# Performance work log

Measured on AMD Instinct MI355X. Metric: run time of the kernel, lower is better.

The kernel has to match this reference:

```python
import jax, jax.numpy as jnp
import numpy as np

N_NODES = 100000
N_EDGES = 1600000
N_FEAT = 128
HIDDEN = 128
N_GRAPHS = 64
N_CLASSES = 10
BN_EPS = 1e-5


def setup_inputs() -> dict:
    key = jax.random.key(0)
    ks = jax.random.split(key, 24)
    glorot = lambda k, o, i: jax.random.normal(k, (o, i), jnp.float32) * (1.0 / np.sqrt(i))
    inp = {
        'x': jax.random.normal(ks[0], (N_NODES, N_FEAT), jnp.float32),
        'edge_index': jax.random.randint(ks[1], (2, N_EDGES), 0, N_NODES, jnp.int64),
        'batch': jnp.sort(jax.random.randint(ks[2], (N_NODES,), 0, N_GRAPHS, jnp.int64)),
        # GCNConv(128 -> 128)
        'gcn_w': glorot(ks[3], HIDDEN, N_FEAT),
        'gcn_b': jnp.zeros((HIDDEN,), jnp.float32),
        # SAGEConv layers 1, 2: lin_l (aggregated, with bias) + lin_r (root, no bias)
        'sage1_wl': glorot(ks[4], HIDDEN, HIDDEN),
        'sage1_bl': jnp.zeros((HIDDEN,), jnp.float32),
        'sage1_wr': glorot(ks[5], HIDDEN, HIDDEN),
        'sage2_wl': glorot(ks[6], HIDDEN, HIDDEN),
        'sage2_bl': jnp.zeros((HIDDEN,), jnp.float32),
        'sage2_wr': glorot(ks[7], HIDDEN, HIDDEN),
        # ClassifierBase: 128 -> 200 -> 100 -> 50 -> 10
        'clf_w0': glorot(ks[8], 200, HIDDEN), 'clf_b0': jnp.zeros((200,), jnp.float32),
        'clf_w1': glorot(ks[9], 100, 200), 'clf_b1': jnp.zeros((100,), jnp.float32),
        'clf_w2': glorot(ks[10], 50, 100), 'clf_b2': jnp.zeros((50,), jnp.float32),
        'clf_w3': glorot(ks[11], N_CLASSES, 50), 'clf_b3': jnp.zeros((N_CLASSES,), jnp.float32),
        # BatchNorm1d (eval mode, running_mean=0, running_var=1)
        'bn0_g': jnp.ones((200,), jnp.float32), 'bn0_b': jnp.zeros((200,), jnp.float32),
        'bn1_g': jnp.ones((100,), jnp.float32), 'bn1_b': jnp.zeros((100,), jnp.float32),
        'bn2_g': jnp.ones((50,), jnp.float32), 'bn2_b': jnp.zeros((50,), jnp.float32),
    }
    return inp


def _gcn_conv(x, src, dst, W, b):
    # PyG GCNConv: add self loops, symmetric deg^{-1/2} normalization
    xw = x @ W.T                                                  # [N, H]
    ones = jnp.ones(src.shape[0], xw.dtype)
    deg = jax.ops.segment_sum(ones, dst, num_segments=N_NODES) + 1.0  # self loops
    dinv = jax.lax.rsqrt(deg)
    norm = dinv[src] * dinv[dst]                                  # [E]
    out = jax.ops.segment_sum(xw[src] * norm[:, None], dst, num_segments=N_NODES)
    out = out + xw * (dinv * dinv)[:, None]                       # self-loop term deg^{-1}
    return out + b


def _sage_conv(x, src, dst, Wl, bl, Wr):
    # PyG SAGEConv (mean aggr): lin_l(mean_{j->i} x_j) + lin_r(x_i)
    ones = jnp.ones(src.shape[0], x.dtype)
    cnt = jax.ops.segment_sum(ones, dst, num_segments=N_NODES)
    agg = jax.ops.segment_sum(x[src], dst, num_segments=N_NODES)
    agg = agg / jnp.maximum(cnt, 1.0)[:, None]
    return agg @ Wl.T + bl + x @ Wr.T


def _bn_eval(h, g, b):
    # eval-mode BatchNorm1d with running_mean=0, running_var=1
    return h * (g / np.sqrt(1.0 + BN_EPS)) + b


def reference(x, edge_index, batch, gcn_w, gcn_b,
              sage1_wl, sage1_bl, sage1_wr, sage2_wl, sage2_bl, sage2_wr,
              clf_w0, clf_b0, clf_w1, clf_b1, clf_w2, clf_b2, clf_w3, clf_b3,
              bn0_g, bn0_b, bn1_g, bn1_b, bn2_g, bn2_b):
    src, dst = edge_index[0], edge_index[1]
    h = _gcn_conv(x, src, dst, gcn_w, gcn_b)          # act_func is None -> no activation
    h = _sage_conv(h, src, dst, sage1_wl, sage1_bl, sage1_wr)
    h = _sage_conv(h, src, dst, sage2_wl, sage2_bl, sage2_wr)
    # global mean pool over graphs
    gcnt = jax.ops.segment_sum(jnp.ones(h.shape[0], h.dtype), batch, num_segments=N_GRAPHS)
    g = jax.ops.segment_sum(h, batch, num_segments=N_GRAPHS) / jnp.maximum(gcnt, 1.0)[:, None]
    # ClassifierBase (eval: dropout inactive), tanh activation
    g = jnp.tanh(_bn_eval(g @ clf_w0.T + clf_b0, bn0_g, bn0_b))
    g = jnp.tanh(_bn_eval(g @ clf_w1.T + clf_b1, bn1_g, bn1_b))
    g = jnp.tanh(_bn_eval(g @ clf_w2.T + clf_b2, bn2_g, bn2_b))
    logits = g @ clf_w3.T + clf_b3
    return jax.nn.softmax(logits, axis=1)             # [B, n_classes]
```

## Files before the change

### kernel.cpp

```cpp
#include <hip/hip_runtime.h>

#define N_NODES 100000
#define N_EDGES 1600000
#define NGRAPH 64
#define NBIN 391
#define EPB 2560
#define NBLK 625
#define CAPB 6144
#define CAPP 7168
#define PSPLIT 8

typedef short s8v __attribute__((ext_vector_type(8)));
typedef float f4v __attribute__((ext_vector_type(4)));
typedef float f2v __attribute__((ext_vector_type(2)));

__device__ __forceinline__ float bflo(unsigned u) { return __uint_as_float(u << 16); }
__device__ __forceinline__ float bfhi(unsigned u) { return __uint_as_float(u & 0xffff0000u); }
__device__ __forceinline__ unsigned short f2bf(float f) {
    unsigned u = __float_as_uint(f);
    u += 0x7fffu + ((u >> 16) & 1u);
    return (unsigned short)(u >> 16);
}
__device__ __forceinline__ float bf2f(unsigned short h) { return __uint_as_float(((unsigned)h) << 16); }
__device__ __forceinline__ unsigned pk(float lo, float hi) {
    return (unsigned)f2bf(lo) | ((unsigned)f2bf(hi) << 16);
}
__device__ __forceinline__ float ldv(const void* p, int i, int f32) {
    return f32 ? ((const float*)p)[i] : bf2f(((const unsigned short*)p)[i]);
}
__device__ __forceinline__ f2v up2(unsigned u) {
    f2v t; t.x = bflo(u); t.y = bfhi(u); return t;
}

__global__ __launch_bounds__(256) void k_setup(const unsigned short* __restrict__ x,
                                               const int* __restrict__ ei,
                                               const int* __restrict__ batch,
                                               int* __restrict__ flags,
                                               int* __restrict__ binCur,
                                               int* __restrict__ gstart,
                                               float* __restrict__ pbuf,
                                               float* __restrict__ wbuf,
                                               const void* w0, const void* w1,
                                               const void* w2, const void* w3,
                                               const void* b0, const void* bn0g, const void* bn0b,
                                               const void* b1, const void* bn1g, const void* bn1b,
                                               const void* b2, const void* bn2g, const void* bn2b,
                                               const void* b3) {
    __shared__ int cnt[3];
    int tid = threadIdx.x, bid = blockIdx.x;
    if (tid < 3) cnt[tid] = 0;
    __syncthreads();
    unsigned short h = x[tid * 37];
    int e = (h >> 7) & 0xFF;
    if (e >= 100 && e <= 150) atomicAdd(&cnt[0], 1);
    if (bid == 0) {
        if (ei[2 * (tid * 5000) + 1] == 0) atomicAdd(&cnt[1], 1);
        if (batch[2 * (tid * 193) + 1] == 0) atomicAdd(&cnt[2], 1);
    }
    __syncthreads();
    int f = (cnt[0] == 256) ? 0 : 1;
    int i = bid * 256 + tid;
    if (i < 25600) wbuf[i] = ldv(w0, i, f);
    else if (i < 45600) wbuf[i] = ldv(w1, i - 25600, f);
    else if (i < 50600) wbuf[i] = ldv(w2, i - 45600, f);
    else if (i < 51100) wbuf[i] = ldv(w3, i - 50600, f);
    if (bid != 0) return;
    int b64 = (cnt[2] == 256) ? 1 : 0;
    if (tid == 0) {
        flags[0] = f;
        flags[1] = (cnt[1] == 256) ? 1 : 0;
        flags[2] = b64;
    }
    for (int k = tid; k < NBIN; k += 256) binCur[k] = k * CAPB;
    if (tid <= NGRAPH) {
        int g = tid, lo = 0, hi = N_NODES;
        while (lo < hi) {
            int mid = (lo + hi) >> 1;
            int v = b64 ? batch[2 * mid] : batch[mid];
            if (v < g) lo = mid + 1;
            else hi = mid;
        }
        gstart[g] = lo;
    }
    const float invs = rsqrtf(1.0f + 1e-5f);
    if (tid < 200) {
        float a = ldv(bn0g, tid, f) * invs;
        pbuf[tid] = a;
        pbuf[200 + tid] = ldv(b0, tid, f) * a + ldv(bn0b, tid, f);
    }
    if (tid < 100) {
        float a = ldv(bn1g, tid, f) * invs;
        pbuf[400 + tid] = a;
        pbuf[500 + tid] = ldv(b1, tid, f) * a + ldv(bn1b, tid, f);
    }
    if (tid < 50) {
        float a = ldv(bn2g, tid, f) * invs;
        pbuf[600 + tid] = a;
        pbuf[650 + tid] = ldv(b2, tid, f) * a + ldv(bn2b, tid, f);
    }
    if (tid < 10) pbuf[700 + tid] = ldv(b3, tid, f);
}

__global__ __launch_bounds__(256) void k_binfill(const int* __restrict__ ei,
                                                 int* __restrict__ binCur,
                                                 unsigned* __restrict__ staging,
                                                 const int* __restrict__ flags) {
    __shared__ int cnt[NBIN];
    __shared__ int lofs[NBIN];
    __shared__ int curL[NBIN];
    __shared__ int basg[NBIN];
    __shared__ int sA[512], sB[512];
    __shared__ int sbuf[EPB];
    __shared__ int dbuf[EPB];
    __shared__ unsigned ebuf[EPB];
    __shared__ unsigned short bbuf[EPB];
    int tid = threadIdx.x;
    int i64 = flags[1];
    int base = blockIdx.x * EPB;
    for (int i = tid; i < NBIN; i += 256) cnt[i] = 0;
    __syncthreads();
    #pragma unroll
    for (int k = 0; k < EPB / 512; ++k) {
        int e = base + k * 512 + tid * 2;
        int s0, s1, d0, d1;
        if (i64) {
            uint4 vs = *(const uint4*)(ei + 2 * (size_t)e);
            uint4 vd = *(const uint4*)(ei + 2 * (size_t)(N_EDGES + e));
            s0 = (int)vs.x; s1 = (int)vs.z;
            d0 = (int)vd.x; d1 = (int)vd.z;
        } else {
            int2 vs = *(const int2*)(ei + (size_t)e);
            int2 vd = *(const int2*)(ei + (size_t)N_EDGES + e);
            s0 = vs.x; s1 = vs.y;
            d0 = vd.x; d1 = vd.y;
        }
        int l = k * 512 + tid * 2;
        sbuf[l] = s0; sbuf[l + 1] = s1;
        dbuf[l] = d0; dbuf[l + 1] = d1;
        if ((unsigned)d0 < N_NODES) atomicAdd(&cnt[d0 >> 8], 1);
        if ((unsigned)d1 < N_NODES) atomicAdd(&cnt[d1 >> 8], 1);
    }
    __syncthreads();
    for (int k = tid; k < 512; k += 256) sA[k] = (k < NBIN) ? cnt[k] : 0;
    __syncthreads();
    int* src = sA;
    int* dst = sB;
    for (int off = 1; off < 512; off <<= 1) {
        for (int k = tid; k < 512; k += 256)
            dst[k] = src[k] + ((k >= off) ? src[k - off] : 0);
        __syncthreads();
        int* t = src; src = dst; dst = t;
    }
    int totE = src[NBIN - 1];
    for (int i = tid; i < NBIN; i += 256) {
        int excl = src[i] - cnt[i];
        lofs[i] = excl;
        curL[i] = excl;
        basg[i] = cnt[i] ? atomicAdd(&binCur[i], cnt[i]) : 0;
    }
    __syncthreads();
    #pragma unroll
    for (int k = 0; k < EPB / 256; ++k) {
        int l = k * 256 + tid;
        int d = dbuf[l];
        int s = sbuf[l];
        if ((unsigned)d < N_NODES) {
            s = min(max(s, 0), N_NODES - 1);
            int p = atomicAdd(&curL[d >> 8], 1);
            ebuf[p] = ((unsigned)(d & 255) << 20) | (unsigned)s;
            bbuf[p] = (unsigned short)(d >> 8);
        }
    }
    __syncthreads();
    for (int i = tid; i < totE; i += 256) {
        int bb = bbuf[i];
        int p = basg[bb] + (i - lofs[bb]);
        if (p < (bb + 1) * CAPB) staging[p] = ebuf[i];
    }
}

__global__ __launch_bounds__(256) void k_csr(const unsigned* __restrict__ staging,
                                             const int* __restrict__ binCur,
                                             int2* __restrict__ rse,
                                             float* __restrict__ dinv,
                                             int* __restrict__ colidx,
                                             unsigned* __restrict__ padA,
                                             unsigned* __restrict__ padB) {
    __shared__ int deg[256];
    __shared__ int s[256];
    __shared__ int cur[256];
    __shared__ int colbuf[CAPP];
    int b = blockIdx.x, tid = threadIdx.x;
    int n0 = b << 8;
    int nend = min(256, N_NODES - n0);
    int runStart = b * CAPB;
    int outStart = b * CAPP;
    int runLen = min(binCur[b] - runStart, CAPB);
    deg[tid] = 0;
    for (int i = tid; i < CAPP; i += 256) colbuf[i] = N_NODES;
    __syncthreads();
    for (int i = tid; i < runLen; i += 256)
        atomicAdd(&deg[staging[runStart + i] >> 20], 1);
    __syncthreads();
    int myDeg = deg[tid];
    int pdeg = (myDeg + 15) & ~15;
    s[tid] = pdeg;
    __syncthreads();
    for (int off = 1; off < 256; off <<= 1) {
        int x2 = (tid >= off) ? s[tid - off] : 0;
        __syncthreads();
        s[tid] += x2;
        __syncthreads();
    }
    int incl = s[tid];
    int lrs = incl - pdeg;
    if (tid < nend) {
        rse[n0 + tid] = make_int2(outStart + lrs, outStart + lrs + myDeg);
        dinv[n0 + tid] = rsqrtf((float)myDeg + 1.0f);
    }
    cur[tid] = lrs;
    __syncthreads();
    for (int i = tid; i < runLen; i += 256) {
        unsigned e = staging[runStart + i];
        int p = atomicAdd(&cur[e >> 20], 1);
        if (p < CAPP) colbuf[p] = (int)(e & 0xFFFFF);
    }
    __syncthreads();
    int ptot = min(s[255], CAPP);
    for (int i = tid; i < ptot; i += 256) colidx[outStart + i] = colbuf[i];
    if (b == 0) {
        if (tid < 64) {
            padA[(size_t)N_NODES * 64 + tid] = 0u;
            padB[(size_t)N_NODES * 64 + tid] = 0u;
        }
        if (tid == 0) dinv[N_NODES] = 0.f;
    }
}

__global__ __launch_bounds__(256) void k_cvtx(const void* __restrict__ src,
                                              unsigned* __restrict__ out,
                                              const int* __restrict__ flags) {
    if (!flags[0]) return;
    int id = blockIdx.x * 256 + threadIdx.x;
    if (id >= N_NODES * 64) return;
    float2 u = ((const float2*)src)[id];
    out[id] = pk(u.x, u.y);
}

template <int MODE>
__global__ __launch_bounds__(256) void k_agg(const uint4* __restrict__ xsA,
                                             const uint4* __restrict__ xsB,
                                             const int2* __restrict__ rse,
                                             const float* __restrict__ dinv,
                                             unsigned* __restrict__ out,
                                             const int* __restrict__ col,
                                             const int* __restrict__ flags) {
    int lane = threadIdx.x & 63;
    int node = blockIdx.x * 4 + (threadIdx.x >> 6);
    int glane = lane & 15, grp = lane >> 4;
    const uint4* xs = (MODE == 0) ? (flags[0] ? xsB : xsA) : xsA;
    int2 rr = rse[node];
    int rs = rr.x, deg = rr.y - rr.x;
    int pend = rs + ((deg + 15) & ~15);
    f2v a0 = {0.f, 0.f}, a1 = {0.f, 0.f}, a2 = {0.f, 0.f}, a3 = {0.f, 0.f};
    uint4 selfu = make_uint4(0u, 0u, 0u, 0u);
    float di = 0.f;
    if (MODE == 0) {
        selfu = xs[(unsigned)node * 16u + glane];
        di = dinv[node];
    }

    for (int base = rs; base < pend; base += 16) {
        int4 c = *(const int4*)(col + base + grp * 4);
        float dv0, dv1, dv2, dv3;
        if (MODE == 0) {
            dv0 = dinv[c.x]; dv1 = dinv[c.y]; dv2 = dinv[c.z]; dv3 = dinv[c.w];
            c.x = min(c.x, N_NODES - 1); c.y = min(c.y, N_NODES - 1);
            c.z = min(c.z, N_NODES - 1); c.w = min(c.w, N_NODES - 1);
        }
        uint4 u0 = xs[(unsigned)c.x * 16u + glane];
        uint4 u1 = xs[(unsigned)c.y * 16u + glane];
        uint4 u2 = xs[(unsigned)c.z * 16u + glane];
        uint4 u3 = xs[(unsigned)c.w * 16u + glane];
        if (MODE == 0) {
            a0 += dv0 * up2(u0.x); a1 += dv0 * up2(u0.y); a2 += dv0 * up2(u0.z); a3 += dv0 * up2(u0.w);
            a0 += dv1 * up2(u1.x); a1 += dv1 * up2(u1.y); a2 += dv1 * up2(u1.z); a3 += dv1 * up2(u1.w);
            a0 += dv2 * up2(u2.x); a1 += dv2 * up2(u2.y); a2 += dv2 * up2(u2.z); a3 += dv2 * up2(u2.w);
            a0 += dv3 * up2(u3.x); a1 += dv3 * up2(u3.y); a2 += dv3 * up2(u3.z); a3 += dv3 * up2(u3.w);
        } else {
            a0 += up2(u0.x); a1 += up2(u0.y); a2 += up2(u0.z); a3 += up2(u0.w);
            a0 += up2(u1.x); a1 += up2(u1.y); a2 += up2(u1.z); a3 += up2(u1.w);
            a0 += up2(u2.x); a1 += up2(u2.y); a2 += up2(u2.z); a3 += up2(u2.w);
            a0 += up2(u3.x); a1 += up2(u3.y); a2 += up2(u3.z); a3 += up2(u3.w);
        }
    }
    float r[8] = {a0.x, a0.y, a1.x, a1.y, a2.x, a2.y, a3.x, a3.y};
    #pragma unroll
    for (int i = 0; i < 8; ++i) {
        float v = r[i];
        v += __shfl_xor(v, 16, 64);
        v += __shfl_xor(v, 32, 64);
        r[i] = v;
    }
    if (MODE == 0) {
        float d2 = di * di;
        r[0] = di * r[0] + d2 * bflo(selfu.x); r[1] = di * r[1] + d2 * bfhi(selfu.x);
        r[2] = di * r[2] + d2 * bflo(selfu.y); r[3] = di * r[3] + d2 * bfhi(selfu.y);
        r[4] = di * r[4] + d2 * bflo(selfu.z); r[5] = di * r[5] + d2 * bfhi(selfu.z);
        r[6] = di * r[6] + d2 * bflo(selfu.w); r[7] = di * r[7] + d2 * bfhi(selfu.w);
    } else {
        float s = 1.0f / fmaxf((float)deg, 1.0f);
        #pragma unroll
        for (int i = 0; i < 8; ++i) r[i] *= s;
    }
    if (grp == 0) {
        uint4 o;
        o.x = pk(r[0], r[1]); o.y = pk(r[2], r[3]);
        o.z = pk(r[4], r[5]); o.w = pk(r[6], r[7]);
        *(uint4*)(out + (size_t)node * 64 + glane * 4) = o;
    }
}

template <int DUAL>
__global__ __launch_bounds__(512) void k_gemm(const unsigned short* A0,
                                              const void* __restrict__ W0,
                                              const unsigned short* __restrict__ A1,
                                              const void* __restrict__ W1,
                                              const void* __restrict__ bias,
                                              unsigned short* out,
                                              const int* __restrict__ flags) {
    __shared__ __align__(16) unsigned short As[128][136];
    __shared__ __align__(16) unsigned short Ws[128][136];
    int f32 = flags[0];
    int tid = threadIdx.x;
    int lane = tid & 63;
    int rowbase = blockIdx.x * 128;
    int lr = lane & 15, q = lane >> 4;
    int m0 = (tid >> 6) * 16;

    f4v acc[8];
    #pragma unroll
    for (int t = 0; t < 8; ++t) acc[t] = (f4v){0.f, 0.f, 0.f, 0.f};

    #pragma unroll
    for (int p = 0; p < (DUAL ? 2 : 1); ++p) {
        const unsigned short* Ap = p ? A1 : A0;
        const void* Wp = p ? W1 : W0;
        if (p) __syncthreads();
        #pragma unroll
        for (int it = 0; it < 4; ++it) {
            int chunk = tid + it * 512;
            int r = chunk >> 4, c8 = (chunk & 15) * 8;
            int grow = rowbase + r;
            uint4 v = make_uint4(0u, 0u, 0u, 0u);
            if (grow < N_NODES) v = *(const uint4*)(Ap + (size_t)grow * 128 + c8);
            *(uint4*)&As[r][c8] = v;
        }
        if (!f32) {
            const unsigned short* Wf = (const unsigned short*)Wp;
            #pragma unroll
            for (int it = 0; it < 4; ++it) {
                int chunk = tid + it * 512;
                int r = chunk >> 4, c8 = (chunk & 15) * 8;
                *(uint4*)&Ws[r][c8] = *(const uint4*)(Wf + r * 128 + c8);
            }
        } else {
            const float* Wf = (const float*)Wp;
            #pragma unroll
            for (int it = 0; it < 8; ++it) {
                int chunk = tid + it * 512;
                int r = chunk >> 5, c4 = (chunk & 31) * 4;
                float4 v = *(const float4*)(Wf + r * 128 + c4);
                unsigned lo = (unsigned)f2bf(v.x) | ((unsigned)f2bf(v.y) << 16);
                unsigned hi = (unsigned)f2bf(v.z) | ((unsigned)f2bf(v.w) << 16);
                *(uint2*)&Ws[r][c4] = make_uint2(lo, hi);
            }
        }
        __syncthreads();
        #pragma unroll
        for (int k = 0; k < 4; ++k) {
            s8v a = *(const s8v*)&As[m0 + lr][k * 32 + q * 8];
            #pragma unroll
            for (int t = 0; t < 8; ++t) {
                s8v b = *(const s8v*)&Ws[t * 16 + lr][k * 32 + q * 8];
                acc[t] = __builtin_amdgcn_mfma_f32_16x16x32_bf16(a, b, acc[t], 0, 0, 0);
            }
        }
    }
    #pragma unroll
    for (int t = 0; t < 8; ++t) {
        int o = t * 16 + lr;
        float bv = ldv(bias, o, f32);
        #pragma unroll
        for (int j = 0; j < 4; ++j) {
            int m = rowbase + m0 + q * 4 + j;
            if (m < N_NODES) out[(size_t)m * 128 + o] = f2bf(acc[t][j] + bv);
        }
    }
}

__global__ __launch_bounds__(256) void k_pool2(const unsigned* __restrict__ h,
                                               const int* __restrict__ gstart,
                                               float* __restrict__ ppool) {
    __shared__ float part[4][128];
    int g = blockIdx.x / PSPLIT, sl = blockIdx.x % PSPLIT;
    int wave = threadIdx.x >> 6, lane = threadIdx.x & 63;
    int s0 = gstart[g], s1 = gstart[g + 1];
    int n = s1 - s0;
    int chunk = (n + PSPLIT - 1) / PSPLIT;
    int r0 = s0 + sl * chunk;
    int r1 = min(r0 + chunk, s1);
    float a0 = 0.f, a1 = 0.f;
    for (int r = r0 + wave; r < r1; r += 4) {
        unsigned u = h[(size_t)r * 64 + lane];
        a0 += bflo(u);
        a1 += bfhi(u);
    }
    part[wave][2 * lane] = a0;
    part[wave][2 * lane + 1] = a1;
    __syncthreads();
    int t = threadIdx.x;
    if (t < 128) {
        float s = part[0][t] + part[1][t] + part[2][t] + part[3][t];
        ppool[(size_t)blockIdx.x * 128 + t] = s;
    }
}

__global__ __launch_bounds__(256) void k_clf(const float* __restrict__ ppool,
                                             const int* __restrict__ gstart,
                                             const float* __restrict__ wbuf,
                                             const float* __restrict__ pbuf,
                                             void* outv, const int* __restrict__ flags) {
    __shared__ float gin[128];
    __shared__ float ha[200];
    __shared__ float hb[100];
    int b = blockIdx.x, t = threadIdx.x;
    if (t < 128) {
        float s = 0.f;
        #pragma unroll
        for (int k = 0; k < PSPLIT; ++k) s += ppool[(size_t)(b * PSPLIT + k) * 128 + t];
        int cnt = gstart[b + 1] - gstart[b];
        gin[t] = s / fmaxf((float)cnt, 1.0f);
    }
    __syncthreads();
    if (t < 200) {
        const float4* wr = (const float4*)(wbuf + t * 128);
        float s = 0.f;
        #pragma unroll
        for (int k = 0; k < 32; ++k) {
            float4 v = wr[k];
            s += v.x * gin[4 * k] + v.y * gin[4 * k + 1] + v.z * gin[4 * k + 2] + v.w * gin[4 * k + 3];
        }
        ha[t] = tanhf(s * pbuf[t] + pbuf[200 + t]);
    }
    __syncthreads();
    if (t < 100) {
        const float4* wr = (const float4*)(wbuf + 25600 + t * 200);
        float s = 0.f;
        #pragma unroll
        for (int k = 0; k < 50; ++k) {
            float4 v = wr[k];
            s += v.x * ha[4 * k] + v.y * ha[4 * k + 1] + v.z * ha[4 * k + 2] + v.w * ha[4 * k + 3];
        }
        hb[t] = tanhf(s * pbuf[400 + t] + pbuf[500 + t]);
    }
    __syncthreads();
    if (t < 50) {
        const float4* wr = (const float4*)(wbuf + 45600 + t * 100);
        float s = 0.f;
        #pragma unroll
        for (int k = 0; k < 25; ++k) {
            float4 v = wr[k];
            s += v.x * hb[4 * k] + v.y * hb[4 * k + 1] + v.z * hb[4 * k + 2] + v.w * hb[4 * k + 3];
        }
        gin[t] = tanhf(s * pbuf[600 + t] + pbuf[650 + t]);
    }
    __syncthreads();
    if (t == 0) {
        int f = flags[0];
        float lg[10];
        float mx = -1e30f;
        #pragma unroll
        for (int c = 0; c < 10; ++c) {
            const float* wr = wbuf + 50600 + c * 50;
            float s = 0.f;
            for (int k = 0; k < 50; ++k) s += wr[k] * gin[k];
            s += pbuf[700 + c];
            lg[c] = s;
            mx = fmaxf(mx, s);
        }
        float sum = 0.f;
        #pragma unroll
        for (int c = 0; c < 10; ++c) {
            lg[c] = __expf(lg[c] - mx);
            sum += lg[c];
        }
        float inv = 1.0f / sum;
        #pragma unroll
        for (int c = 0; c < 10; ++c) {
            float v = lg[c] * inv;
            if (f) ((float*)outv)[b * 10 + c] = v;
            else ((unsigned short*)outv)[b * 10 + c] = f2bf(v);
        }
    }
}

extern "C" void kernel_launch(void* const* d_in, const int* in_sizes, int n_in,
                              void* d_out, int out_size, void* d_ws, size_t ws_size,
                              hipStream_t stream) {
    const unsigned short* x16 = (const unsigned short*)d_in[0];
    const int* ei = (const int*)d_in[1];
    const int* batch = (const int*)d_in[2];

    char* ws = (char*)d_ws;
    size_t off = 0;
    auto alloc = [&](size_t bytes) {
        size_t r = off;
        off = (off + bytes + 255) & ~(size_t)255;
        return r;
    };
    int* flags = (int*)(ws + alloc(256));
    int2* rse = (int2*)(ws + alloc((size_t)N_NODES * 8));
    int* colidx = (int*)(ws + alloc((size_t)NBIN * CAPP * 4));
    float* dinv = (float*)(ws + alloc((size_t)(N_NODES + 1) * 4));
    int* binCur = (int*)(ws + alloc(NBIN * 4));
    int* gstart = (int*)(ws + alloc((NGRAPH + 1) * 4));
    float* pbuf = (float*)(ws + alloc(710 * 4));
    float* ppool = (float*)(ws + alloc((size_t)NGRAPH * PSPLIT * 128 * 4));
    float* wbuf = (float*)(ws + alloc(51100 * 4));
    unsigned short* bufA = (unsigned short*)(ws + alloc((size_t)(N_NODES + 1) * 128 * 2));
    unsigned short* bufB = (unsigned short*)(ws + alloc((size_t)(N_NODES + 1) * 128 * 2));
    unsigned* staging = (unsigned*)bufA;

    k_setup<<<200, 256, 0, stream>>>(x16, ei, batch, flags, binCur, gstart, pbuf, wbuf,
                                     d_in[11], d_in[13], d_in[15], d_in[17],
                                     d_in[12], d_in[19], d_in[20],
                                     d_in[14], d_in[21], d_in[22],
                                     d_in[16], d_in[23], d_in[24], d_in[18]);

    k_binfill<<<NBLK, 256, 0, stream>>>(ei, binCur, staging, flags);
    k_csr<<<NBIN, 256, 0, stream>>>(staging, binCur, rse, dinv, colidx,
                                    (unsigned*)bufA, (unsigned*)bufB);
    k_cvtx<<<(N_NODES * 64 + 255) / 256, 256, 0, stream>>>((const void*)x16,
                                                           (unsigned*)bufB, flags);

    k_agg<0><<<N_NODES / 4, 256, 0, stream>>>((const uint4*)x16, (const uint4*)bufB,
                                              rse, dinv, (unsigned*)bufA, colidx, flags);
    k_gemm<0><<<(N_NODES + 127) / 128, 512, 0, stream>>>(bufA, d_in[3], nullptr, nullptr,
                                                         d_in[4], bufA, flags);
    k_agg<1><<<N_NODES / 4, 256, 0, stream>>>((const uint4*)bufA, (const uint4*)bufA,
                                              rse, dinv, (unsigned*)bufB, colidx, flags);
    k_gemm<1><<<(N_NODES + 127) / 128, 512, 0, stream>>>(bufB, d_in[5], bufA, d_in[7],
                                                         d_in[6], bufB, flags);
    k_agg<1><<<N_NODES / 4, 256, 0, stream>>>((const uint4*)bufB, (const uint4*)bufB,
                                              rse, dinv, (unsigned*)bufA, colidx, flags);
    k_gemm<1><<<(N_NODES + 127) / 128, 512, 0, stream>>>(bufA, d_in[8], bufB, d_in[10],
                                                         d_in[9], bufA, flags);
    k_pool2<<<NGRAPH * PSPLIT, 256, 0, stream>>>((const unsigned*)bufA, gstart, ppool);
    k_clf<<<NGRAPH, 256, 0, stream>>>(ppool, gstart, wbuf, pbuf, d_out, flags);
}
```

Measured before the change: 473.2 us.

## Fuse neighbor aggregation with the following GEMM into one kernel per layer

```diff
diff --git a/kernel.cpp b/kernel.cpp
--- a/kernel.cpp
+++ b/kernel.cpp
@@ -247,117 +247,181 @@
     out[id] = pk(u.x, u.y);
 }
 
+__device__ __forceinline__ void accrow(f2v* a, uint4 u, float w, bool weighted) {
+    if (weighted) {
+        a[0] += up2(u.x) * w; a[1] += up2(u.y) * w;
+        a[2] += up2(u.z) * w; a[3] += up2(u.w) * w;
+    } else {
+        a[0] += up2(u.x); a[1] += up2(u.y);
+        a[2] += up2(u.z); a[3] += up2(u.w);
+    }
+}
+
 template <int MODE>
-__global__ __launch_bounds__(256) void k_agg(const uint4* __restrict__ xsA,
-                                             const uint4* __restrict__ xsB,
-                                             const int2* __restrict__ rse,
-                                             const float* __restrict__ dinv,
-                                             unsigned* __restrict__ out,
-                                             const int* __restrict__ col,
-                                             const int* __restrict__ flags) {
-    int lane = threadIdx.x & 63;
-    int node = blockIdx.x * 4 + (threadIdx.x >> 6);
-    int glane = lane & 15, grp = lane >> 4;
-    const uint4* xs = (MODE == 0) ? (flags[0] ? xsB : xsA) : xsA;
-    int2 rr = rse[node];
-    int rs = rr.x, deg = rr.y - rr.x;
-    int pend = rs + ((deg + 15) & ~15);
-    f2v a0 = {0.f, 0.f}, a1 = {0.f, 0.f}, a2 = {0.f, 0.f}, a3 = {0.f, 0.f};
-    uint4 selfu = make_uint4(0u, 0u, 0u, 0u);
-    float di = 0.f;
-    if (MODE == 0) {
-        selfu = xs[(unsigned)node * 16u + glane];
-        di = dinv[node];
-    }
-
-    for (int base = rs; base < pend; base += 16) {
-        int4 c = *(const int4*)(col + base + grp * 4);
-        float dv0, dv1, dv2, dv3;
-        if (MODE == 0) {
-            dv0 = dinv[c.x]; dv1 = dinv[c.y]; dv2 = dinv[c.z]; dv3 = dinv[c.w];
-            c.x = min(c.x, N_NODES - 1); c.y = min(c.y, N_NODES - 1);
-            c.z = min(c.z, N_NODES - 1); c.w = min(c.w, N_NODES - 1);
-        }
-        uint4 u0 = xs[(unsigned)c.x * 16u + glane];
-        uint4 u1 = xs[(unsigned)c.y * 16u + glane];
-        uint4 u2 = xs[(unsigned)c.z * 16u + glane];
-        uint4 u3 = xs[(unsigned)c.w * 16u + glane];
-        if (MODE == 0) {
-            a0 += dv0 * up2(u0.x); a1 += dv0 * up2(u0.y); a2 += dv0 * up2(u0.z); a3 += dv0 * up2(u0.w);
-            a0 += dv1 * up2(u1.x); a1 += dv1 * up2(u1.y); a2 += dv1 * up2(u1.z); a3 += dv1 * up2(u1.w);
-            a0 += dv2 * up2(u2.x); a1 += dv2 * up2(u2.y); a2 += dv2 * up2(u2.z); a3 += dv2 * up2(u2.w);
-            a0 += dv3 * up2(u3.x); a1 += dv3 * up2(u3.y); a2 += dv3 * up2(u3.z); a3 += dv3 * up2(u3.w);
-        } else {
-            a0 += up2(u0.x); a1 += up2(u0.y); a2 += up2(u0.z); a3 += up2(u0.w);
-            a0 += up2(u1.x); a1 += up2(u1.y); a2 += up2(u1.z); a3 += up2(u1.w);
-            a0 += up2(u2.x); a1 += up2(u2.y); a2 += up2(u2.z); a3 += up2(u2.w);
-            a0 += up2(u3.x); a1 += up2(u3.y); a2 += up2(u3.z); a3 += up2(u3.w);
-        }
-    }
-    float r[8] = {a0.x, a0.y, a1.x, a1.y, a2.x, a2.y, a3.x, a3.y};
-    #pragma unroll
-    for (int i = 0; i < 8; ++i) {
-        float v = r[i];
-        v += __shfl_xor(v, 16, 64);
-        v += __shfl_xor(v, 32, 64);
-        r[i] = v;
-    }
-    if (MODE == 0) {
-        float d2 = di * di;
-        r[0] = di * r[0] + d2 * bflo(selfu.x); r[1] = di * r[1] + d2 * bfhi(selfu.x);
-        r[2] = di * r[2] + d2 * bflo(selfu.y); r[3] = di * r[3] + d2 * bfhi(selfu.y);
-        r[4] = di * r[4] + d2 * bflo(selfu.z); r[5] = di * r[5] + d2 * bfhi(selfu.z);
-        r[6] = di * r[6] + d2 * bflo(selfu.w); r[7] = di * r[7] + d2 * bfhi(selfu.w);
-    } else {
-        float s = 1.0f / fmaxf((float)deg, 1.0f);
-        #pragma unroll
-        for (int i = 0; i < 8; ++i) r[i] *= s;
-    }
-    if (grp == 0) {
-        uint4 o;
-        o.x = pk(r[0], r[1]); o.y = pk(r[2], r[3]);
-        o.z = pk(r[4], r[5]); o.w = pk(r[6], r[7]);
-        *(uint4*)(out + (size_t)node * 64 + glane * 4) = o;
-    }
-}
-
-template <int DUAL>
-__global__ __launch_bounds__(512) void k_gemm(const unsigned short* A0,
-                                              const void* __restrict__ W0,
-                                              const unsigned short* __restrict__ A1,
-                                              const void* __restrict__ W1,
-                                              const void* __restrict__ bias,
-                                              unsigned short* out,
-                                              const int* __restrict__ flags) {
+__global__ __launch_bounds__(512) void k_aggemm(const uint4* __restrict__ xsA,
+                                                const uint4* __restrict__ xsB,
+                                                const void* __restrict__ W0,
+                                                const void* __restrict__ W1,
+                                                const void* __restrict__ bias,
+                                                const int2* __restrict__ rse,
+                                                const float* __restrict__ dinv,
+                                                const int* __restrict__ col,
+                                                unsigned short* __restrict__ out,
+                                                const int* __restrict__ flags) {
     __shared__ __align__(16) unsigned short As[128][136];
     __shared__ __align__(16) unsigned short Ws[128][136];
     int f32 = flags[0];
+    const uint4* xs = (MODE == 0) ? (f32 ? xsB : xsA) : xsA;
     int tid = threadIdx.x;
-    int lane = tid & 63;
+    int wave = tid >> 6, lane = tid & 63;
+    int glane = lane & 15, grp = lane >> 4;
     int rowbase = blockIdx.x * 128;
-    int lr = lane & 15, q = lane >> 4;
-    int m0 = (tid >> 6) * 16;
-
+
+    if (!f32) {
+        const unsigned short* Wf = (const unsigned short*)W0;
+        #pragma unroll
+        for (int it = 0; it < 4; ++it) {
+            int chunk = tid + it * 512;
+            int r = chunk >> 4, c8 = (chunk & 15) * 8;
+            *(uint4*)&Ws[r][c8] = *(const uint4*)(Wf + r * 128 + c8);
+        }
+    } else {
+        const float* Wf = (const float*)W0;
+        #pragma unroll
+        for (int it = 0; it < 8; ++it) {
+            int chunk = tid + it * 512;
+            int r = chunk >> 5, c4 = (chunk & 31) * 4;
+            float4 v = *(const float4*)(Wf + r * 128 + c4);
+            *(uint2*)&Ws[r][c4] = make_uint2(pk(v.x, v.y), pk(v.z, v.w));
+        }
+    }
+
+    for (int nd = 0; nd < 16; nd += 2) {
+        int nodeA = rowbase + wave * 16 + nd;
+        int nodeB = nodeA + 1;
+        int okA = nodeA < N_NODES, okB = nodeB < N_NODES;
+        int2 ra = rse[okA ? nodeA : 0];
+        int2 rb = rse[okB ? nodeB : 0];
+        int degA = okA ? ra.y - ra.x : 0;
+        int degB = okB ? rb.y - rb.x : 0;
+        int pdA = (degA + 15) & ~15, pdB = (degB + 15) & ~15;
+        int pendA = ra.x + pdA, pendB = rb.x + pdB;
+        int rounds = max(pdA, pdB) >> 4;
+        int baseA = ra.x + grp * 4, baseB = rb.x + grp * 4;
+        f2v accA[4], accB[4];
+        #pragma unroll
+        for (int j = 0; j < 4; ++j) { accA[j] = (f2v){0.f, 0.f}; accB[j] = (f2v){0.f, 0.f}; }
+
+        for (int r = 0; r < rounds; ++r) {
+            int4 ca = *(const int4*)(col + baseA);
+            int4 cb = *(const int4*)(col + baseB);
+            int mA = baseA < pendA, mB = baseB < pendB;
+            ca.x = mA ? ca.x : N_NODES; ca.y = mA ? ca.y : N_NODES;
+            ca.z = mA ? ca.z : N_NODES; ca.w = mA ? ca.w : N_NODES;
+            cb.x = mB ? cb.x : N_NODES; cb.y = mB ? cb.y : N_NODES;
+            cb.z = mB ? cb.z : N_NODES; cb.w = mB ? cb.w : N_NODES;
+            float dA0 = 0.f, dA1 = 0.f, dA2 = 0.f, dA3 = 0.f;
+            float dB0 = 0.f, dB1 = 0.f, dB2 = 0.f, dB3 = 0.f;
+            if (MODE == 0) {
+                dA0 = dinv[ca.x]; dA1 = dinv[ca.y]; dA2 = dinv[ca.z]; dA3 = dinv[ca.w];
+                dB0 = dinv[cb.x]; dB1 = dinv[cb.y]; dB2 = dinv[cb.z]; dB3 = dinv[cb.w];
+                ca.x = min(ca.x, N_NODES - 1); ca.y = min(ca.y, N_NODES - 1);
+                ca.z = min(ca.z, N_NODES - 1); ca.w = min(ca.w, N_NODES - 1);
+                cb.x = min(cb.x, N_NODES - 1); cb.y = min(cb.y, N_NODES - 1);
+                cb.z = min(cb.z, N_NODES - 1); cb.w = min(cb.w, N_NODES - 1);
+            }
+            uint4 u0 = xs[(size_t)(unsigned)ca.x * 16u + glane];
+            uint4 u1 = xs[(size_t)(unsigned)ca.y * 16u + glane];
+            uint4 u2 = xs[(size_t)(unsigned)ca.z * 16u + glane];
+            uint4 u3 = xs[(size_t)(unsigned)ca.w * 16u + glane];
+            uint4 v0 = xs[(size_t)(unsigned)cb.x * 16u + glane];
+            uint4 v1 = xs[(size_t)(unsigned)cb.y * 16u + glane];
+            uint4 v2 = xs[(size_t)(unsigned)cb.z * 16u + glane];
+            uint4 v3 = xs[(size_t)(unsigned)cb.w * 16u + glane];
+            accrow(accA, u0, dA0, MODE == 0);
+            accrow(accA, u1, dA1, MODE == 0);
+            accrow(accA, u2, dA2, MODE == 0);
+            accrow(accA, u3, dA3, MODE == 0);
+            accrow(accB, v0, dB0, MODE == 0);
+            accrow(accB, v1, dB1, MODE == 0);
+            accrow(accB, v2, dB2, MODE == 0);
+            accrow(accB, v3, dB3, MODE == 0);
+            baseA += 16; baseB += 16;
+        }
+        float rA[8] = {accA[0].x, accA[0].y, accA[1].x, accA[1].y,
+                       accA[2].x, accA[2].y, accA[3].x, accA[3].y};
+        float rB[8] = {accB[0].x, accB[0].y, accB[1].x, accB[1].y,
+                       accB[2].x, accB[2].y, accB[3].x, accB[3].y};
+        #pragma unroll
+        for (int i = 0; i < 8; ++i) {
+            float v = rA[i];
+            v += __shfl_xor(v, 16, 64);
+            v += __shfl_xor(v, 32, 64);
+            rA[i] = v;
+            float w = rB[i];
+            w += __shfl_xor(w, 16, 64);
+            w += __shfl_xor(w, 32, 64);
+            rB[i] = w;
+        }
+        if (MODE == 0) {
+            uint4 z = make_uint4(0u, 0u, 0u, 0u);
+            uint4 sa = okA ? xs[(size_t)nodeA * 16u + glane] : z;
+            uint4 sb = okB ? xs[(size_t)nodeB * 16u + glane] : z;
+            float diA = dinv[okA ? nodeA : 0], dA2s = diA * diA;
+            float diB = dinv[okB ? nodeB : 0], dB2s = diB * diB;
+            rA[0] = diA * rA[0] + dA2s * bflo(sa.x); rA[1] = diA * rA[1] + dA2s * bfhi(sa.x);
+            rA[2] = diA * rA[2] + dA2s * bflo(sa.y); rA[3] = diA * rA[3] + dA2s * bfhi(sa.y);
+            rA[4] = diA * rA[4] + dA2s * bflo(sa.z); rA[5] = diA * rA[5] + dA2s * bfhi(sa.z);
+            rA[6] = diA * rA[6] + dA2s * bflo(sa.w); rA[7] = diA * rA[7] + dA2s * bfhi(sa.w);
+            rB[0] = diB * rB[0] + dB2s * bflo(sb.x); rB[1] = diB * rB[1] + dB2s * bfhi(sb.x);
+            rB[2] = diB * rB[2] + dB2s * bflo(sb.y); rB[3] = diB * rB[3] + dB2s * bfhi(sb.y);
+            rB[4] = diB * rB[4] + dB2s * bflo(sb.z); rB[5] = diB * rB[5] + dB2s * bfhi(sb.z);
+            rB[6] = diB * rB[6] + dB2s * bflo(sb.w); rB[7] = diB * rB[7] + dB2s * bfhi(sb.w);
+        } else {
+            float sA = 1.0f / fmaxf((float)degA, 1.0f);
+            float sB = 1.0f / fmaxf((float)degB, 1.0f);
+            #pragma unroll
+            for (int i = 0; i < 8; ++i) { rA[i] *= sA; rB[i] *= sB; }
+        }
+        if (grp == 0) {
+            uint4 o;
+            o.x = pk(rA[0], rA[1]); o.y = pk(rA[2], rA[3]);
+            o.z = pk(rA[4], rA[5]); o.w = pk(rA[6], rA[7]);
+            *(uint4*)&As[wave * 16 + nd][glane * 8] = o;
+            o.x = pk(rB[0], rB[1]); o.y = pk(rB[2], rB[3]);
+            o.z = pk(rB[4], rB[5]); o.w = pk(rB[6], rB[7]);
+            *(uint4*)&As[wave * 16 + nd + 1][glane * 8] = o;
+        }
+    }
+    __syncthreads();
+
+    int lr = glane, q = grp;
+    int m0 = wave * 16;
     f4v acc[8];
     #pragma unroll
     for (int t = 0; t < 8; ++t) acc[t] = (f4v){0.f, 0.f, 0.f, 0.f};
-
     #pragma unroll
-    for (int p = 0; p < (DUAL ? 2 : 1); ++p) {
-        const unsigned short* Ap = p ? A1 : A0;
-        const void* Wp = p ? W1 : W0;
-        if (p) __syncthreads();
+    for (int k = 0; k < 4; ++k) {
+        s8v a = *(const s8v*)&As[m0 + lr][k * 32 + q * 8];
+        #pragma unroll
+        for (int t = 0; t < 8; ++t) {
+            s8v b = *(const s8v*)&Ws[t * 16 + lr][k * 32 + q * 8];
+            acc[t] = __builtin_amdgcn_mfma_f32_16x16x32_bf16(a, b, acc[t], 0, 0, 0);
+        }
+    }
+    if (MODE == 1) {
+        __syncthreads();
         #pragma unroll
         for (int it = 0; it < 4; ++it) {
             int chunk = tid + it * 512;
-            int r = chunk >> 4, c8 = (chunk & 15) * 8;
+            int r = chunk >> 4, c8i = chunk & 15;
             int grow = rowbase + r;
             uint4 v = make_uint4(0u, 0u, 0u, 0u);
-            if (grow < N_NODES) v = *(const uint4*)(Ap + (size_t)grow * 128 + c8);
-            *(uint4*)&As[r][c8] = v;
+            if (grow < N_NODES) v = xs[(size_t)grow * 16u + c8i];
+            *(uint4*)&As[r][c8i * 8] = v;
         }
         if (!f32) {
-            const unsigned short* Wf = (const unsigned short*)Wp;
+            const unsigned short* Wf = (const unsigned short*)W1;
             #pragma unroll
             for (int it = 0; it < 4; ++it) {
                 int chunk = tid + it * 512;
@@ -365,15 +429,13 @@
                 *(uint4*)&Ws[r][c8] = *(const uint4*)(Wf + r * 128 + c8);
             }
         } else {
-            const float* Wf = (const float*)Wp;
+            const float* Wf = (const float*)W1;
             #pragma unroll
             for (int it = 0; it < 8; ++it) {
                 int chunk = tid + it * 512;
                 int r = chunk >> 5, c4 = (chunk & 31) * 4;
                 float4 v = *(const float4*)(Wf + r * 128 + c4);
-                unsigned lo = (unsigned)f2bf(v.x) | ((unsigned)f2bf(v.y) << 16);
-                unsigned hi = (unsigned)f2bf(v.z) | ((unsigned)f2bf(v.w) << 16);
-                *(uint2*)&Ws[r][c4] = make_uint2(lo, hi);
+                *(uint2*)&Ws[r][c4] = make_uint2(pk(v.x, v.y), pk(v.z, v.w));
             }
         }
         __syncthreads();
@@ -521,7 +583,7 @@
     };
     int* flags = (int*)(ws + alloc(256));
     int2* rse = (int2*)(ws + alloc((size_t)N_NODES * 8));
-    int* colidx = (int*)(ws + alloc((size_t)NBIN * CAPP * 4));
+    int* colidx = (int*)(ws + alloc((size_t)NBIN * CAPP * 4 + 4096));
     float* dinv = (float*)(ws + alloc((size_t)(N_NODES + 1) * 4));
     int* binCur = (int*)(ws + alloc(NBIN * 4));
     int* gstart = (int*)(ws + alloc((NGRAPH + 1) * 4));
@@ -544,18 +606,16 @@
     k_cvtx<<<(N_NODES * 64 + 255) / 256, 256, 0, stream>>>((const void*)x16,
                                                            (unsigned*)bufB, flags);
 
-    k_agg<0><<<N_NODES / 4, 256, 0, stream>>>((const uint4*)x16, (const uint4*)bufB,
-                                              rse, dinv, (unsigned*)bufA, colidx, flags);
-    k_gemm<0><<<(N_NODES + 127) / 128, 512, 0, stream>>>(bufA, d_in[3], nullptr, nullptr,
-                                                         d_in[4], bufA, flags);
-    k_agg<1><<<N_NODES / 4, 256, 0, stream>>>((const uint4*)bufA, (const uint4*)bufA,
-                                              rse, dinv, (unsigned*)bufB, colidx, flags);
-    k_gemm<1><<<(N_NODES + 127) / 128, 512, 0, stream>>>(bufB, d_in[5], bufA, d_in[7],
-                                                         d_in[6], bufB, flags);
-    k_agg<1><<<N_NODES / 4, 256, 0, stream>>>((const uint4*)bufB, (const uint4*)bufB,
-                                              rse, dinv, (unsigned*)bufA, colidx, flags);
-    k_gemm<1><<<(N_NODES + 127) / 128, 512, 0, stream>>>(bufA, d_in[8], bufB, d_in[10],
-                                                         d_in[9], bufA, flags);
+    const int NLBLK = (N_NODES + 127) / 128;
+    k_aggemm<0><<<NLBLK, 512, 0, stream>>>((const uint4*)x16, (const uint4*)bufB,
+                                           d_in[3], nullptr, d_in[4],
+                                           rse, dinv, colidx, bufA, flags);
+    k_aggemm<1><<<NLBLK, 512, 0, stream>>>((const uint4*)bufA, nullptr,
+                                           d_in[5], d_in[7], d_in[6],
+                                           rse, dinv, colidx, bufB, flags);
+    k_aggemm<1><<<NLBLK, 512, 0, stream>>>((const uint4*)bufB, nullptr,
+                                           d_in[8], d_in[10], d_in[9],
+                                           rse, dinv, colidx, bufA, flags);
     k_pool2<<<NGRAPH * PSPLIT, 256, 0, stream>>>((const unsigned*)bufA, gstart, ppool);
     k_clf<<<NGRAPH, 256, 0, stream>>>(ppool, gstart, wbuf, pbuf, d_out, flags);
 }
```

Result: slower. 507.9 us (+7.3%).

## Fold x conversion into setup kernel and load GEMM A operand directly to registers

Applied to the files above, without the earlier changes.

```diff
diff --git a/kernel.cpp b/kernel.cpp
--- a/kernel.cpp
+++ b/kernel.cpp
@@ -9,6 +9,7 @@
 #define CAPB 6144
 #define CAPP 7168
 #define PSPLIT 8
+#define SETUPBLK 1600
 
 typedef short s8v __attribute__((ext_vector_type(8)));
 typedef float f4v __attribute__((ext_vector_type(4)));
@@ -40,6 +41,7 @@
                                                int* __restrict__ gstart,
                                                float* __restrict__ pbuf,
                                                float* __restrict__ wbuf,
+                                               unsigned* __restrict__ xcvt,
                                                const void* w0, const void* w1,
                                                const void* w2, const void* w3,
                                                const void* b0, const void* bn0g, const void* bn0b,
@@ -64,6 +66,12 @@
     else if (i < 45600) wbuf[i] = ldv(w1, i - 25600, f);
     else if (i < 50600) wbuf[i] = ldv(w2, i - 45600, f);
     else if (i < 51100) wbuf[i] = ldv(w3, i - 50600, f);
+    if (f) {
+        for (int id = bid * 256 + tid; id < N_NODES * 64; id += SETUPBLK * 256) {
+            float2 u = ((const float2*)x)[id];
+            xcvt[id] = pk(u.x, u.y);
+        }
+    }
     if (bid != 0) return;
     int b64 = (cnt[2] == 256) ? 1 : 0;
     if (tid == 0) {
@@ -235,16 +243,6 @@
         }
         if (tid == 0) dinv[N_NODES] = 0.f;
     }
-}
-
-__global__ __launch_bounds__(256) void k_cvtx(const void* __restrict__ src,
-                                              unsigned* __restrict__ out,
-                                              const int* __restrict__ flags) {
-    if (!flags[0]) return;
-    int id = blockIdx.x * 256 + threadIdx.x;
-    if (id >= N_NODES * 64) return;
-    float2 u = ((const float2*)src)[id];
-    out[id] = pk(u.x, u.y);
 }
 
 template <int MODE>
@@ -322,21 +320,23 @@
 }
 
 template <int DUAL>
-__global__ __launch_bounds__(512) void k_gemm(const unsigned short* A0,
+__global__ __launch_bounds__(512) void k_gemm(const unsigned short* __restrict__ A0,
                                               const void* __restrict__ W0,
                                               const unsigned short* __restrict__ A1,
                                               const void* __restrict__ W1,
                                               const void* __restrict__ bias,
-                                              unsigned short* out,
+                                              unsigned short* __restrict__ out,
                                               const int* __restrict__ flags) {
-    __shared__ __align__(16) unsigned short As[128][136];
     __shared__ __align__(16) unsigned short Ws[128][136];
     int f32 = flags[0];
     int tid = threadIdx.x;
     int lane = tid & 63;
+    int wave = tid >> 6;
     int rowbase = blockIdx.x * 128;
     int lr = lane & 15, q = lane >> 4;
-    int m0 = (tid >> 6) * 16;
+    int m0 = wave * 16;
+    int arow = rowbase + m0 + lr;
+    if (arow > N_NODES) arow = N_NODES;
 
     f4v acc[8];
     #pragma unroll
@@ -347,15 +347,6 @@
         const unsigned short* Ap = p ? A1 : A0;
         const void* Wp = p ? W1 : W0;
         if (p) __syncthreads();
-        #pragma unroll
-        for (int it = 0; it < 4; ++it) {
-            int chunk = tid + it * 512;
-            int r = chunk >> 4, c8 = (chunk & 15) * 8;
-            int grow = rowbase + r;
-            uint4 v = make_uint4(0u, 0u, 0u, 0u);
-            if (grow < N_NODES) v = *(const uint4*)(Ap + (size_t)grow * 128 + c8);
-            *(uint4*)&As[r][c8] = v;
-        }
         if (!f32) {
             const unsigned short* Wf = (const unsigned short*)Wp;
             #pragma unroll
@@ -371,19 +362,20 @@
                 int chunk = tid + it * 512;
                 int r = chunk >> 5, c4 = (chunk & 31) * 4;
                 float4 v = *(const float4*)(Wf + r * 128 + c4);
-                unsigned lo = (unsigned)f2bf(v.x) | ((unsigned)f2bf(v.y) << 16);
-                unsigned hi = (unsigned)f2bf(v.z) | ((unsigned)f2bf(v.w) << 16);
-                *(uint2*)&Ws[r][c4] = make_uint2(lo, hi);
+                *(uint2*)&Ws[r][c4] = make_uint2(pk(v.x, v.y), pk(v.z, v.w));
             }
         }
+        const unsigned short* Arp = Ap + (size_t)arow * 128;
+        s8v a[4];
+        #pragma unroll
+        for (int k = 0; k < 4; ++k) a[k] = *(const s8v*)(Arp + k * 32 + q * 8);
         __syncthreads();
         #pragma unroll
         for (int k = 0; k < 4; ++k) {
-            s8v a = *(const s8v*)&As[m0 + lr][k * 32 + q * 8];
             #pragma unroll
             for (int t = 0; t < 8; ++t) {
                 s8v b = *(const s8v*)&Ws[t * 16 + lr][k * 32 + q * 8];
-                acc[t] = __builtin_amdgcn_mfma_f32_16x16x32_bf16(a, b, acc[t], 0, 0, 0);
+                acc[t] = __builtin_amdgcn_mfma_f32_16x16x32_bf16(a[k], b, acc[t], 0, 0, 0);
             }
         }
     }
@@ -521,7 +513,7 @@
     };
     int* flags = (int*)(ws + alloc(256));
     int2* rse = (int2*)(ws + alloc((size_t)N_NODES * 8));
-    int* colidx = (int*)(ws + alloc((size_t)NBIN * CAPP * 4));
+    int* colidx = (int*)(ws + alloc((size_t)NBIN * CAPP * 4 + 4096));
     float* dinv = (float*)(ws + alloc((size_t)(N_NODES + 1) * 4));
     int* binCur = (int*)(ws + alloc(NBIN * 4));
     int* gstart = (int*)(ws + alloc((NGRAPH + 1) * 4));
@@ -532,17 +524,16 @@
     unsigned short* bufB = (unsigned short*)(ws + alloc((size_t)(N_NODES + 1) * 128 * 2));
     unsigned* staging = (unsigned*)bufA;
 
-    k_setup<<<200, 256, 0, stream>>>(x16, ei, batch, flags, binCur, gstart, pbuf, wbuf,
-                                     d_in[11], d_in[13], d_in[15], d_in[17],
-                                     d_in[12], d_in[19], d_in[20],
-                                     d_in[14], d_in[21], d_in[22],
-                                     d_in[16], d_in[23], d_in[24], d_in[18]);
+    k_setup<<<SETUPBLK, 256, 0, stream>>>(x16, ei, batch, flags, binCur, gstart, pbuf, wbuf,
+                                          (unsigned*)bufB,
+                                          d_in[11], d_in[13], d_in[15], d_in[17],
+                                          d_in[12], d_in[19], d_in[20],
+                                          d_in[14], d_in[21], d_in[22],
+                                          d_in[16], d_in[23], d_in[24], d_in[18]);
 
     k_binfill<<<NBLK, 256, 0, stream>>>(ei, binCur, staging, flags);
     k_csr<<<NBIN, 256, 0, stream>>>(staging, binCur, rse, dinv, colidx,
                                     (unsigned*)bufA, (unsigned*)bufB);
-    k_cvtx<<<(N_NODES * 64 + 255) / 256, 256, 0, stream>>>((const void*)x16,
-                                                           (unsigned*)bufB, flags);
 
     k_agg<0><<<N_NODES / 4, 256, 0, stream>>>((const uint4*)x16, (const uint4*)bufB,
                                               rse, dinv, (unsigned*)bufA, colidx, flags);
```

New measurement: 460.5 us. 2.7% less time.
